# Kernel tuning notes

Measured on AMD Instinct MI355X. Metric: run time of the kernel, lower is better.

Reference implementation:

```python
import jax, jax.numpy as jnp
import numpy as np

BN_EPS = 1e-5


def setup_inputs() -> dict:
    key = jax.random.key(0)
    ks = jax.random.split(key, 6)
    B, N, M, C1, C2 = 8, 8192, 2048, 128, 256
    in_ch = C1 + C2  # 384
    return {
        "xyz1": jax.random.uniform(ks[0], (B, N, 3), dtype=jnp.float32),
        "xyz2": jax.random.uniform(ks[1], (B, M, 3), dtype=jnp.float32),
        "features1": jax.random.normal(ks[2], (B, C1, N), dtype=jnp.float32),
        "features2": jax.random.normal(ks[3], (B, C2, M), dtype=jnp.float32),
        # Conv1d(kernel_size=1, bias=False) weights, squeezed to [out, in]
        "conv_w0": jax.random.normal(ks[4], (256, in_ch), dtype=jnp.float32) * 0.05,
        "gamma0": jnp.ones((256,), dtype=jnp.float32),
        "beta0": jnp.zeros((256,), dtype=jnp.float32),
        "conv_w1": jax.random.normal(ks[5], (256, 256), dtype=jnp.float32) * 0.05,
        "gamma1": jnp.ones((256,), dtype=jnp.float32),
        "beta1": jnp.zeros((256,), dtype=jnp.float32),
    }


def _conv_bn_relu(x, w, gamma, beta):
    # 1x1 Conv1d (no bias) == per-point channel matmul: [B,Cin,N] -> [B,Cout,N]
    x = jnp.einsum("oc,bcn->bon", w, x)
    # BatchNorm1d in training mode: batch stats over (B, N), biased variance
    mu = jnp.mean(x, axis=(0, 2), keepdims=True)
    var = jnp.var(x, axis=(0, 2), keepdims=True)
    x = (x - mu) * jax.lax.rsqrt(var + BN_EPS)
    x = x * gamma[None, :, None] + beta[None, :, None]
    return jax.nn.relu(x)


def reference(xyz1, xyz2, features1, features2,
              conv_w0, gamma0, beta0, conv_w1, gamma1, beta1):
    # squared pairwise distances [B, N, M] (broadcast diff reduced over coord dim)
    diff = xyz1[:, :, None, :] - xyz2[:, None, :, :]  # [B,N,M,3]
    dists = jnp.sum(diff * diff, axis=-1)             # [B,N,M]
    idx = jnp.argmin(dists, axis=-1)                  # [B,N] nearest downsampled point

    # per-batch gather: features2[b, :, idx[b]] -> [B, C2, N]
    interp = jax.vmap(lambda f, i: f[:, i])(features2, idx)

    x = jnp.concatenate([features1, interp], axis=1)  # [B, C1+C2, N]
    x = _conv_bn_relu(x, conv_w0, gamma0, beta0)
    x = _conv_bn_relu(x, conv_w1, gamma1, beta1)
    return x
```

## Files before the change

kernel.cpp:

```cpp
#include <hip/hip_runtime.h>
#include <stdint.h>

typedef unsigned short u16;
typedef unsigned int u32;
typedef __attribute__((ext_vector_type(8))) short short8;
typedef __attribute__((ext_vector_type(4))) float floatx4;

__device__ __forceinline__ u16 f2b(float f) {
  union { float f; u32 u; } c; c.f = f;
  u32 u = c.u;
  u += 0x7fffu + ((u >> 16) & 1u);
  return (u16)(u >> 16);
}
__device__ __forceinline__ float b2f(u16 h) {
  union { u32 u; float f; } c; c.u = ((u32)h) << 16;
  return c.f;
}

__device__ __forceinline__ void glds16(const void* g, void* l) {
  __builtin_amdgcn_global_load_lds((__attribute__((address_space(1))) void*)g,
                                   (__attribute__((address_space(3))) void*)l, 16, 0, 0);
}

__global__ void prep_all_k(const float* __restrict__ xyz1, const float* __restrict__ xyz2,
                           float2* __restrict__ cand,
                           const float* __restrict__ f1, u16* __restrict__ f1t,
                           const float* __restrict__ f2, u16* __restrict__ f2t,
                           const float* __restrict__ w0, u16* __restrict__ w0b,
                           const float* __restrict__ w1, u16* __restrict__ w1b,
                           float* __restrict__ sums) {
  __shared__ __align__(16) char smem[9216];
  int blk = blockIdx.x, t = threadIdx.x;
  if (blk < 512) {
    float4* s2 = (float4*)smem;
    int nq = blk & 7, mq = (blk >> 3) & 7, b = blk >> 6;
    const float* x2 = xyz2 + ((size_t)b * 2048 + mq * 256) * 3;
    s2[t] = make_float4(x2[t * 3], x2[t * 3 + 1], x2[t * 3 + 2], 0.f);
    __syncthreads();
    int n0 = nq * 1024 + t;
    float px[4], py[4], pz[4];
#pragma unroll
    for (int q = 0; q < 4; q++) {
      const float* p1 = xyz1 + ((size_t)b * 8192 + n0 + q * 256) * 3;
      px[q] = p1[0]; py[q] = p1[1]; pz[q] = p1[2];
    }
    float best[4] = {3.0e38f, 3.0e38f, 3.0e38f, 3.0e38f};
    int bi[4] = {0, 0, 0, 0};
#pragma unroll 4
    for (int m = 0; m < 256; m++) {
      float4 qq = s2[m];
#pragma unroll
      for (int q = 0; q < 4; q++) {
        float dx = px[q] - qq.x, dy = py[q] - qq.y, dz = pz[q] - qq.z;
        float d = fmaf(dz, dz, fmaf(dy, dy, dx * dx));
        bool c = d < best[q];
        best[q] = c ? d : best[q];
        bi[q] = c ? m : bi[q];
      }
    }
#pragma unroll
    for (int q = 0; q < 4; q++) {
      int n = n0 + q * 256;
      cand[(size_t)mq * 65536 + (size_t)b * 8192 + n] =
          make_float2(best[q], __int_as_float(mq * 256 + bi[q]));
    }
  } else if (blk < 3584) {
    const float* in; u16* out; int C, N, bx, by, bz;
    if (blk < 2560) { int rel = blk - 512;  in = f1; out = f1t; C = 128; N = 8192; bx = rel & 127; by = (rel >> 7) & 1; bz = rel >> 8; }
    else            { int rel = blk - 2560; in = f2; out = f2t; C = 256; N = 2048; bx = rel & 31;  by = (rel >> 5) & 3; bz = rel >> 7; }
    u16 (*tile)[72] = (u16(*)[72])smem;
    int c0 = by * 64, n0 = bx * 64;
    const float* src = in + ((size_t)bz * C + c0) * N + n0;
#pragma unroll
    for (int i = 0; i < 4; i++) {
      int id = t + i * 256;
      int c = id >> 4, nq = (id & 15) * 4;
      float4 v = *(const float4*)(src + (size_t)c * N + nq);
      tile[nq + 0][c] = f2b(v.x);
      tile[nq + 1][c] = f2b(v.y);
      tile[nq + 2][c] = f2b(v.z);
      tile[nq + 3][c] = f2b(v.w);
    }
    __syncthreads();
    int n = t >> 2, ch = (t & 3) * 16;
    u16* dst = out + ((size_t)bz * N + n0 + n) * C + c0 + ch;
    *(uint4*)dst = *(const uint4*)&tile[n][ch];
    *(uint4*)(dst + 8) = *(const uint4*)&tile[n][ch + 8];
  } else {
    int rel = blk - 3584;
    int i = rel * 256 + t;
    if (rel < 384) w0b[i] = f2b(w0[i]);
    else { int j = i - 98304; w1b[j] = f2b(w1[j]); }
    if (rel < 4) sums[i] = 0.f;
  }
}

__global__ __launch_bounds__(256, 4) void gemm1_k(const u16* __restrict__ w0b, const u16* __restrict__ f1t,
                                                  const u16* __restrict__ f2t, const float2* __restrict__ cand,
                                                  float* __restrict__ sum0, float* __restrict__ sq0,
                                                  u16* __restrict__ y0) {
  __shared__ u16 As[128 * 64];
  __shared__ u16 Bs[128 * 64];
  __shared__ int sidx[128];
  int t = threadIdx.x;
  int ot = blockIdx.x & 1;
  int pt0 = (blockIdx.x >> 1) * 128;
  int o0 = ot * 128;
  int b = pt0 >> 13;
  if (t < 128) {
    int p = pt0 + t;
    float bd = 3.0e38f; int bi = 0;
#pragma unroll
    for (int qc = 0; qc < 8; qc++) {
      float2 c = cand[(size_t)qc * 65536 + p];
      if (c.x < bd) { bd = c.x; bi = __float_as_int(c.y); }
    }
    sidx[t] = bi;
  }
  floatx4 zero = {0.f, 0.f, 0.f, 0.f};
  floatx4 acc[4][4];
#pragma unroll
  for (int i = 0; i < 4; i++)
#pragma unroll
    for (int j = 0; j < 4; j++) acc[i][j] = zero;
  int lane = t & 63, wave = t >> 6;
  int wrow = (wave >> 1) * 64, wcol = (wave & 1) * 64;
  int lr = lane & 15, lq = lane >> 4;
  int srow = lane >> 3;
  int sch = ((lane & 7) ^ srow) * 8;
  __syncthreads();
  int prow[4], gidx[4];
#pragma unroll
  for (int i = 0; i < 4; i++) {
    prow[i] = (wave * 4 + i) * 8 + srow;
    gidx[i] = sidx[prow[i]];
  }

#pragma unroll
  for (int k0 = 0; k0 < 384; k0 += 64) {
    __syncthreads();
#pragma unroll
    for (int i = 0; i < 4; i++) {
      int chunk = wave * 4 + i;
      glds16(w0b + (size_t)(o0 + chunk * 8 + srow) * 384 + k0 + sch, &As[chunk * 512]);
    }
    if (k0 < 128) {
#pragma unroll
      for (int i = 0; i < 4; i++)
        glds16(f1t + (size_t)(pt0 + prow[i]) * 128 + k0 + sch, &Bs[(wave * 4 + i) * 512]);
    } else {
#pragma unroll
      for (int i = 0; i < 4; i++)
        glds16(f2t + ((size_t)(b << 11) + gidx[i]) * 256 + (k0 - 128) + sch, &Bs[(wave * 4 + i) * 512]);
    }
    __syncthreads();
#pragma unroll
    for (int ks = 0; ks < 2; ks++) {
      short8 af[4], bf[4];
#pragma unroll
      for (int i = 0; i < 4; i++) {
        int row = wrow + i * 16 + lr;
        af[i] = *(const short8*)&As[row * 64 + ((((ks << 2) | lq) ^ (lr & 7)) << 3)];
      }
#pragma unroll
      for (int j = 0; j < 4; j++) {
        int row = wcol + j * 16 + lr;
        bf[j] = *(const short8*)&Bs[row * 64 + ((((ks << 2) | lq) ^ (lr & 7)) << 3)];
      }
#pragma unroll
      for (int i = 0; i < 4; i++)
#pragma unroll
        for (int j = 0; j < 4; j++)
          acc[i][j] = __builtin_amdgcn_mfma_f32_16x16x32_bf16(af[i], bf[j], acc[i][j], 0, 0, 0);
    }
  }
#pragma unroll
  for (int i = 0; i < 4; i++) {
#pragma unroll
    for (int j = 0; j < 4; j++) {
      int o = o0 + wrow + i * 16 + lq * 4;
      int p = pt0 + wcol + j * 16 + lr;
      uint2 pk;
      pk.x = (u32)f2b(acc[i][j][0]) | ((u32)f2b(acc[i][j][1]) << 16);
      pk.y = (u32)f2b(acc[i][j][2]) | ((u32)f2b(acc[i][j][3]) << 16);
      *(uint2*)&y0[(size_t)p * 256 + o] = pk;
    }
  }
  __syncthreads();
  float* red = (float*)As;
  red[t] = 0.f;
  __syncthreads();
#pragma unroll
  for (int i = 0; i < 4; i++) {
#pragma unroll
    for (int r = 0; r < 4; r++) {
      float s = acc[i][0][r] + acc[i][1][r] + acc[i][2][r] + acc[i][3][r];
      float q = acc[i][0][r] * acc[i][0][r] + acc[i][1][r] * acc[i][1][r] +
                acc[i][2][r] * acc[i][2][r] + acc[i][3][r] * acc[i][3][r];
#pragma unroll
      for (int m = 8; m >= 1; m >>= 1) { s += __shfl_xor(s, m); q += __shfl_xor(q, m); }
      if (lr == 0) {
        int o = wrow + i * 16 + lq * 4 + r;
        atomicAdd(&red[o], s);
        atomicAdd(&red[128 + o], q);
      }
    }
  }
  __syncthreads();
  if (t < 128) {
    atomicAdd(&sum0[o0 + t], red[t]);
    atomicAdd(&sq0[o0 + t], red[128 + t]);
  }
}

__global__ __launch_bounds__(256, 4) void gemm2_k(const u16* __restrict__ w1b, const u16* __restrict__ y0,
                                                  const float* __restrict__ sum0, const float* __restrict__ sq0,
                                                  const float* __restrict__ gamma0, const float* __restrict__ beta0,
                                                  float* __restrict__ sum1, float* __restrict__ sq1,
                                                  u16* __restrict__ y1) {
  __shared__ u16 As[128 * 64];
  __shared__ u16 Bs[128 * 72];
  __shared__ float ssc[256], ssh[256];
  int t = threadIdx.x;
  {
    float mean = sum0[t] * (1.f / 65536.f);
    float var = fmaxf(sq0[t] * (1.f / 65536.f) - mean * mean, 0.f);
    float r = rsqrtf(var + 1e-5f);
    float sc = gamma0[t] * r;
    ssc[t] = sc;
    ssh[t] = beta0[t] - mean * sc;
  }
  int ot = blockIdx.x & 1;
  int pt0 = (blockIdx.x >> 1) * 128;
  int o0 = ot * 128;
  floatx4 zero = {0.f, 0.f, 0.f, 0.f};
  floatx4 acc[4][4];
#pragma unroll
  for (int i = 0; i < 4; i++)
#pragma unroll
    for (int j = 0; j < 4; j++) acc[i][j] = zero;
  int lane = t & 63, wave = t >> 6;
  int wrow = (wave >> 1) * 64, wcol = (wave & 1) * 64;
  int lr = lane & 15, lq = lane >> 4;
  int srow = lane >> 3;
  int sch = ((lane & 7) ^ srow) * 8;

#pragma unroll
  for (int k0 = 0; k0 < 256; k0 += 64) {
    __syncthreads();
#pragma unroll
    for (int i = 0; i < 4; i++) {
      int chunk = wave * 4 + i;
      glds16(w1b + (size_t)(o0 + chunk * 8 + srow) * 256 + k0 + sch, &As[chunk * 512]);
    }
#pragma unroll
    for (int i = 0; i < 4; i++) {
      int id = t + i * 256;
      int row = id >> 3, ch = (id & 7) * 8;
      uint4 raw = *(const uint4*)(y0 + (size_t)(pt0 + row) * 256 + k0 + ch);
      u32 rw[4] = {raw.x, raw.y, raw.z, raw.w};
      u32 ow[4];
#pragma unroll
      for (int w = 0; w < 4; w++) {
        int k = k0 + ch + w * 2;
        float v0 = b2f((u16)(rw[w] & 0xffffu));
        float v1 = b2f((u16)(rw[w] >> 16));
        v0 = fmaxf(v0 * ssc[k] + ssh[k], 0.f);
        v1 = fmaxf(v1 * ssc[k + 1] + ssh[k + 1], 0.f);
        ow[w] = (u32)f2b(v0) | ((u32)f2b(v1) << 16);
      }
      uint4 ov; ov.x = ow[0]; ov.y = ow[1]; ov.z = ow[2]; ov.w = ow[3];
      *(uint4*)&Bs[row * 72 + ch] = ov;
    }
    __syncthreads();
#pragma unroll
    for (int ks = 0; ks < 2; ks++) {
      int kk = ks * 32 + lq * 8;
      short8 af[4], bf[4];
#pragma unroll
      for (int i = 0; i < 4; i++) {
        int row = wrow + i * 16 + lr;
        af[i] = *(const short8*)&As[row * 64 + ((((ks << 2) | lq) ^ (lr & 7)) << 3)];
      }
#pragma unroll
      for (int j = 0; j < 4; j++) bf[j] = *(const short8*)&Bs[(wcol + j * 16 + lr) * 72 + kk];
#pragma unroll
      for (int i = 0; i < 4; i++)
#pragma unroll
        for (int j = 0; j < 4; j++)
          acc[i][j] = __builtin_amdgcn_mfma_f32_16x16x32_bf16(af[i], bf[j], acc[i][j], 0, 0, 0);
    }
  }
#pragma unroll
  for (int i = 0; i < 4; i++) {
#pragma unroll
    for (int j = 0; j < 4; j++) {
      int o = o0 + wrow + i * 16 + lq * 4;
      int p = pt0 + wcol + j * 16 + lr;
      uint2 pk;
      pk.x = (u32)f2b(acc[i][j][0]) | ((u32)f2b(acc[i][j][1]) << 16);
      pk.y = (u32)f2b(acc[i][j][2]) | ((u32)f2b(acc[i][j][3]) << 16);
      *(uint2*)&y1[(size_t)p * 256 + o] = pk;
    }
  }
  __syncthreads();
  float* red = (float*)As;
  red[t] = 0.f;
  __syncthreads();
#pragma unroll
  for (int i = 0; i < 4; i++) {
#pragma unroll
    for (int r = 0; r < 4; r++) {
      float s = acc[i][0][r] + acc[i][1][r] + acc[i][2][r] + acc[i][3][r];
      float q = acc[i][0][r] * acc[i][0][r] + acc[i][1][r] * acc[i][1][r] +
                acc[i][2][r] * acc[i][2][r] + acc[i][3][r] * acc[i][3][r];
#pragma unroll
      for (int m = 8; m >= 1; m >>= 1) { s += __shfl_xor(s, m); q += __shfl_xor(q, m); }
      if (lr == 0) {
        int o = wrow + i * 16 + lq * 4 + r;
        atomicAdd(&red[o], s);
        atomicAdd(&red[128 + o], q);
      }
    }
  }
  __syncthreads();
  if (t < 128) {
    atomicAdd(&sum1[o0 + t], red[t]);
    atomicAdd(&sq1[o0 + t], red[128 + t]);
  }
}

__global__ void finalize_k(const u16* __restrict__ y1, const float* __restrict__ sum1,
                           const float* __restrict__ sq1, const float* __restrict__ gamma1,
                           const float* __restrict__ beta1, float* __restrict__ out) {
  __shared__ float tile[64][65];
  __shared__ float fs[64], fh[64];
  int b = blockIdx.z, o0 = blockIdx.y * 64, n0 = blockIdx.x * 64;
  int t = threadIdx.x;
  if (t < 64) {
    int o = o0 + t;
    float mean = sum1[o] * (1.f / 65536.f);
    float var = fmaxf(sq1[o] * (1.f / 65536.f) - mean * mean, 0.f);
    float r = rsqrtf(var + 1e-5f);
    float sc = gamma1[o] * r;
    fs[t] = sc;
    fh[t] = beta1[o] - mean * sc;
  }
  __syncthreads();
  int pl = t >> 2, ch = (t & 3) * 16;
  const u16* src = y1 + ((size_t)(b * 8192 + n0 + pl)) * 256 + o0 + ch;
  uint4 r0 = *(const uint4*)src;
  uint4 r1 = *(const uint4*)(src + 8);
  u16 hv[16];
  *(uint4*)&hv[0] = r0;
  *(uint4*)&hv[8] = r1;
#pragma unroll
  for (int e = 0; e < 16; e++) {
    float v = b2f(hv[e]) * fs[ch + e] + fh[ch + e];
    tile[pl][ch + e] = fmaxf(v, 0.f);
  }
  __syncthreads();
  int ol = t >> 2, nch = (t & 3) * 16;
  float* dst = out + ((size_t)(b * 256 + o0 + ol)) * 8192 + n0 + nch;
#pragma unroll
  for (int j = 0; j < 16; j += 4) {
    float4 v = make_float4(tile[nch + j][ol], tile[nch + j + 1][ol],
                           tile[nch + j + 2][ol], tile[nch + j + 3][ol]);
    *(float4*)(dst + j) = v;
  }
}

extern "C" void kernel_launch(void* const* d_in, const int* in_sizes, int n_in,
                              void* d_out, int out_size, void* d_ws, size_t ws_size,
                              hipStream_t stream) {
  const float* xyz1      = (const float*)d_in[0];
  const float* xyz2      = (const float*)d_in[1];
  const float* features1 = (const float*)d_in[2];
  const float* features2 = (const float*)d_in[3];
  const float* conv_w0   = (const float*)d_in[4];
  const float* gamma0    = (const float*)d_in[5];
  const float* beta0     = (const float*)d_in[6];
  const float* conv_w1   = (const float*)d_in[7];
  const float* gamma1    = (const float*)d_in[8];
  const float* beta1     = (const float*)d_in[9];
  float* out = (float*)d_out;

  char* ws = (char*)d_ws;
  size_t off = 0;
  auto alloc = [&](size_t bytes) {
    char* p = ws + off;
    off = (off + bytes + 4095) & ~(size_t)4095;
    return p;
  };
  float*  sums = (float*)alloc(4 * 256 * 4);
  u16*    w0b  = (u16*)alloc(256 * 384 * 2);
  u16*    w1b  = (u16*)alloc(256 * 256 * 2);
  float2* cand = (float2*)alloc((size_t)8 * 65536 * 8);
  u16*    f1t  = (u16*)alloc((size_t)65536 * 128 * 2);
  u16*    f2t  = (u16*)alloc((size_t)16384 * 256 * 2);
  u16*    y0   = (u16*)alloc((size_t)65536 * 256 * 2);
  u16*    y1   = (u16*)alloc((size_t)65536 * 256 * 2);

  prep_all_k<<<dim3(4224), 256, 0, stream>>>(xyz1, xyz2, cand, features1, f1t,
                                             features2, f2t, conv_w0, w0b, conv_w1, w1b, sums);
  gemm1_k<<<dim3(1024), 256, 0, stream>>>(w0b, f1t, f2t, cand, sums + 0, sums + 256, y0);
  gemm2_k<<<dim3(1024), 256, 0, stream>>>(w1b, y0, sums + 0, sums + 256, gamma0, beta0,
                                          sums + 512, sums + 768, y1);
  finalize_k<<<dim3(128, 4, 8), 256, 0, stream>>>(y1, sums + 512, sums + 768, gamma1, beta1, out);
}
```

Measured before the change: 239.3 us.

## Keep weight slice resident in LDS and loop blocks over point tiles with double buffering

Both GEMM kernels now load their full 128-row weight slice into LDS once per block and iterate over several point tiles (persistent-style, 256 blocks of 512 threads), so weights are no longer re-fetched for every K step of every tile. B tiles are double-buffered so the next K slice loads while the current one computes, and in gemm2 the BN+ReLU transform of y0 is split into register prefetch and LDS write to overlap with MFMA. BN partial sums are accumulated in registers across tiles and reduced once per block, which cuts atomics. The costs are large LDS use (about 128 KB in gemm2), which limits occupancy, and only 256 blocks, which may underfill the device.

```diff
diff --git a/kernel.cpp b/kernel.cpp
--- a/kernel.cpp
+++ b/kernel.cpp
@@ -95,116 +95,148 @@
   }
 }
 
-__global__ __launch_bounds__(256, 4) void gemm1_k(const u16* __restrict__ w0b, const u16* __restrict__ f1t,
+__global__ __launch_bounds__(512, 2) void gemm1_k(const u16* __restrict__ w0b, const u16* __restrict__ f1t,
                                                   const u16* __restrict__ f2t, const float2* __restrict__ cand,
                                                   float* __restrict__ sum0, float* __restrict__ sq0,
                                                   u16* __restrict__ y0) {
-  __shared__ u16 As[128 * 64];
-  __shared__ u16 Bs[128 * 64];
-  __shared__ int sidx[128];
+  __shared__ u16 Aw[128 * 384];
+  __shared__ u16 Bs[2][128 * 64];
   int t = threadIdx.x;
-  int ot = blockIdx.x & 1;
-  int pt0 = (blockIdx.x >> 1) * 128;
-  int o0 = ot * 128;
-  int b = pt0 >> 13;
-  if (t < 128) {
-    int p = pt0 + t;
-    float bd = 3.0e38f; int bi = 0;
-#pragma unroll
-    for (int qc = 0; qc < 8; qc++) {
-      float2 c = cand[(size_t)qc * 65536 + p];
-      if (c.x < bd) { bd = c.x; bi = __float_as_int(c.y); }
-    }
-    sidx[t] = bi;
-  }
-  floatx4 zero = {0.f, 0.f, 0.f, 0.f};
-  floatx4 acc[4][4];
-#pragma unroll
-  for (int i = 0; i < 4; i++)
-#pragma unroll
-    for (int j = 0; j < 4; j++) acc[i][j] = zero;
+  int bid = blockIdx.x;
+  int ohalf = (bid >> 3) & 1;
+  int pairidx = (bid & 7) | ((bid >> 4) << 3);
+  int o0 = ohalf * 128;
   int lane = t & 63, wave = t >> 6;
-  int wrow = (wave >> 1) * 64, wcol = (wave & 1) * 64;
+  int wrow = (wave >> 2) * 64;
+  int wp = (wave & 3) * 32;
   int lr = lane & 15, lq = lane >> 4;
   int srow = lane >> 3;
   int sch = ((lane & 7) ^ srow) * 8;
-  __syncthreads();
-  int prow[4], gidx[4];
-#pragma unroll
-  for (int i = 0; i < 4; i++) {
-    prow[i] = (wave * 4 + i) * 8 + srow;
-    gidx[i] = sidx[prow[i]];
-  }
-
-#pragma unroll
-  for (int k0 = 0; k0 < 384; k0 += 64) {
+
+#pragma unroll
+  for (int it = 0; it < 12; it++) {
+    u32 off = (u32)it * 8192 + (u32)t * 16;
+    int row = off / 768;
+    int c16 = (off - row * 768) >> 4;
+    glds16(w0b + (size_t)(o0 + row) * 384 + ((c16 ^ (row & 7)) << 3),
+           (char*)Aw + (size_t)it * 8192 + (size_t)wave * 1024);
+  }
+
+  float sa[4][4], qa[4][4];
+#pragma unroll
+  for (int i = 0; i < 4; i++)
+#pragma unroll
+    for (int r = 0; r < 4; r++) { sa[i][r] = 0.f; qa[i][r] = 0.f; }
+
+  for (int s = 0; s < 4; s++) {
+    int pt = pairidx * 4 + s;
+    int pt0 = pt * 128;
+    int b = pt0 >> 13;
+    int gidx[2];
+#pragma unroll
+    for (int i = 0; i < 2; i++) {
+      int p = pt0 + (wave * 2 + i) * 8 + srow;
+      float bd = 3.0e38f; int bi = 0;
+#pragma unroll
+      for (int qc = 0; qc < 8; qc++) {
+        float2 c = cand[(size_t)qc * 65536 + p];
+        if (c.x < bd) { bd = c.x; bi = __float_as_int(c.y); }
+      }
+      gidx[i] = bi;
+    }
+    floatx4 zero = {0.f, 0.f, 0.f, 0.f};
+    floatx4 acc[4][2];
+#pragma unroll
+    for (int i = 0; i < 4; i++)
+#pragma unroll
+      for (int j = 0; j < 2; j++) acc[i][j] = zero;
+
+    auto stageB = [&](int k0, int bufi) {
+      if (k0 < 128) {
+#pragma unroll
+        for (int i = 0; i < 2; i++)
+          glds16(f1t + (size_t)(pt0 + (wave * 2 + i) * 8 + srow) * 128 + k0 + sch,
+                 &Bs[bufi][(wave * 2 + i) * 512]);
+      } else {
+#pragma unroll
+        for (int i = 0; i < 2; i++)
+          glds16(f2t + ((size_t)(b << 11) + gidx[i]) * 256 + (k0 - 128) + sch,
+                 &Bs[bufi][(wave * 2 + i) * 512]);
+      }
+    };
+    auto compute = [&](int k0, int bufi) {
+#pragma unroll
+      for (int ks = 0; ks < 2; ks++) {
+        short8 af[4], bf[2];
+#pragma unroll
+        for (int i = 0; i < 4; i++) {
+          int row = wrow + i * 16 + lr;
+          af[i] = *(const short8*)&Aw[row * 384 + ((((k0 >> 3) + (ks << 2) + lq) ^ (lr & 7)) << 3)];
+        }
+#pragma unroll
+        for (int j = 0; j < 2; j++) {
+          int row = wp + j * 16 + lr;
+          bf[j] = *(const short8*)&Bs[bufi][row * 64 + ((((ks << 2) | lq) ^ (lr & 7)) << 3)];
+        }
+#pragma unroll
+        for (int i = 0; i < 4; i++)
+#pragma unroll
+          for (int j = 0; j < 2; j++)
+            acc[i][j] = __builtin_amdgcn_mfma_f32_16x16x32_bf16(af[i], bf[j], acc[i][j], 0, 0, 0);
+      }
+    };
+
+    stageB(0, 0);
     __syncthreads();
 #pragma unroll
+    for (int k0i = 0; k0i < 6; k0i++) {
+      if (k0i < 5) stageB((k0i + 1) * 64, (k0i + 1) & 1);
+      compute(k0i * 64, k0i & 1);
+      __syncthreads();
+    }
+
+#pragma unroll
     for (int i = 0; i < 4; i++) {
-      int chunk = wave * 4 + i;
-      glds16(w0b + (size_t)(o0 + chunk * 8 + srow) * 384 + k0 + sch, &As[chunk * 512]);
-    }
-    if (k0 < 128) {
-#pragma unroll
-      for (int i = 0; i < 4; i++)
-        glds16(f1t + (size_t)(pt0 + prow[i]) * 128 + k0 + sch, &Bs[(wave * 4 + i) * 512]);
-    } else {
-#pragma unroll
-      for (int i = 0; i < 4; i++)
-        glds16(f2t + ((size_t)(b << 11) + gidx[i]) * 256 + (k0 - 128) + sch, &Bs[(wave * 4 + i) * 512]);
-    }
-    __syncthreads();
-#pragma unroll
-    for (int ks = 0; ks < 2; ks++) {
-      short8 af[4], bf[4];
-#pragma unroll
-      for (int i = 0; i < 4; i++) {
-        int row = wrow + i * 16 + lr;
-        af[i] = *(const short8*)&As[row * 64 + ((((ks << 2) | lq) ^ (lr & 7)) << 3)];
-      }
-#pragma unroll
-      for (int j = 0; j < 4; j++) {
-        int row = wcol + j * 16 + lr;
-        bf[j] = *(const short8*)&Bs[row * 64 + ((((ks << 2) | lq) ^ (lr & 7)) << 3)];
-      }
-#pragma unroll
-      for (int i = 0; i < 4; i++)
-#pragma unroll
-        for (int j = 0; j < 4; j++)
-          acc[i][j] = __builtin_amdgcn_mfma_f32_16x16x32_bf16(af[i], bf[j], acc[i][j], 0, 0, 0);
-    }
-  }
-#pragma unroll
-  for (int i = 0; i < 4; i++) {
-#pragma unroll
-    for (int j = 0; j < 4; j++) {
-      int o = o0 + wrow + i * 16 + lq * 4;
-      int p = pt0 + wcol + j * 16 + lr;
-      uint2 pk;
-      pk.x = (u32)f2b(acc[i][j][0]) | ((u32)f2b(acc[i][j][1]) << 16);
-      pk.y = (u32)f2b(acc[i][j][2]) | ((u32)f2b(acc[i][j][3]) << 16);
-      *(uint2*)&y0[(size_t)p * 256 + o] = pk;
-    }
-  }
-  __syncthreads();
-  float* red = (float*)As;
-  red[t] = 0.f;
-  __syncthreads();
-#pragma unroll
-  for (int i = 0; i < 4; i++) {
-#pragma unroll
-    for (int r = 0; r < 4; r++) {
-      float s = acc[i][0][r] + acc[i][1][r] + acc[i][2][r] + acc[i][3][r];
-      float q = acc[i][0][r] * acc[i][0][r] + acc[i][1][r] * acc[i][1][r] +
-                acc[i][2][r] * acc[i][2][r] + acc[i][3][r] * acc[i][3][r];
-#pragma unroll
-      for (int m = 8; m >= 1; m >>= 1) { s += __shfl_xor(s, m); q += __shfl_xor(q, m); }
-      if (lr == 0) {
+#pragma unroll
+      for (int j = 0; j < 2; j++) {
+        int o = o0 + wrow + i * 16 + lq * 4;
+        int p = pt0 + wp + j * 16 + lr;
+        uint2 pk;
+        pk.x = (u32)f2b(acc[i][j][0]) | ((u32)f2b(acc[i][j][1]) << 16);
+        pk.y = (u32)f2b(acc[i][j][2]) | ((u32)f2b(acc[i][j][3]) << 16);
+        *(uint2*)&y0[(size_t)p * 256 + o] = pk;
+      }
+#pragma unroll
+      for (int r = 0; r < 4; r++) {
+        float v0 = acc[i][0][r], v1 = acc[i][1][r];
+        sa[i][r] += v0 + v1;
+        qa[i][r] += v0 * v0 + v1 * v1;
+      }
+    }
+  }
+
+#pragma unroll
+  for (int i = 0; i < 4; i++)
+#pragma unroll
+    for (int r = 0; r < 4; r++)
+#pragma unroll
+      for (int m = 8; m >= 1; m >>= 1) {
+        sa[i][r] += __shfl_xor(sa[i][r], m);
+        qa[i][r] += __shfl_xor(qa[i][r], m);
+      }
+  __syncthreads();
+  float* red = (float*)&Bs[0][0];
+  if (t < 256) red[t] = 0.f;
+  __syncthreads();
+  if (lr == 0) {
+#pragma unroll
+    for (int i = 0; i < 4; i++)
+#pragma unroll
+      for (int r = 0; r < 4; r++) {
         int o = wrow + i * 16 + lq * 4 + r;
-        atomicAdd(&red[o], s);
-        atomicAdd(&red[128 + o], q);
-      }
-    }
+        atomicAdd(&red[o], sa[i][r]);
+        atomicAdd(&red[128 + o], qa[i][r]);
+      }
   }
   __syncthreads();
   if (t < 128) {
@@ -213,16 +245,24 @@
   }
 }
 
-__global__ __launch_bounds__(256, 4) void gemm2_k(const u16* __restrict__ w1b, const u16* __restrict__ y0,
+__global__ __launch_bounds__(512, 2) void gemm2_k(const u16* __restrict__ w1b, const u16* __restrict__ y0,
                                                   const float* __restrict__ sum0, const float* __restrict__ sq0,
                                                   const float* __restrict__ gamma0, const float* __restrict__ beta0,
                                                   float* __restrict__ sum1, float* __restrict__ sq1,
                                                   u16* __restrict__ y1) {
-  __shared__ u16 As[128 * 64];
-  __shared__ u16 Bs[128 * 72];
+  __shared__ u16 Aw[128 * 256];
+  __shared__ u16 Bs[2][256 * 64];
   __shared__ float ssc[256], ssh[256];
   int t = threadIdx.x;
-  {
+  int bid = blockIdx.x;
+  int ohalf = (bid >> 3) & 1;
+  int pairidx = (bid & 7) | ((bid >> 4) << 3);
+  int o0 = ohalf * 128;
+  int lane = t & 63, wave = t >> 6;
+  int wrow = (wave >> 2) * 64;
+  int wp = (wave & 3) * 64;
+  int lr = lane & 15, lq = lane >> 4;
+  if (t < 256) {
     float mean = sum0[t] * (1.f / 65536.f);
     float var = fmaxf(sq0[t] * (1.f / 65536.f) - mean * mean, 0.f);
     float r = rsqrtf(var + 1e-5f);
@@ -230,98 +270,139 @@
     ssc[t] = sc;
     ssh[t] = beta0[t] - mean * sc;
   }
-  int ot = blockIdx.x & 1;
-  int pt0 = (blockIdx.x >> 1) * 128;
-  int o0 = ot * 128;
-  floatx4 zero = {0.f, 0.f, 0.f, 0.f};
-  floatx4 acc[4][4];
+#pragma unroll
+  for (int it = 0; it < 8; it++) {
+    u32 off = (u32)it * 8192 + (u32)t * 16;
+    int row = off >> 9;
+    int c16 = (off & 511) >> 4;
+    glds16(w1b + (size_t)(o0 + row) * 256 + ((c16 ^ (row & 7)) << 3),
+           (char*)Aw + (size_t)it * 8192 + (size_t)wave * 1024);
+  }
+
+  int brow[4], bpc[4], bch[4];
+#pragma unroll
+  for (int i = 0; i < 4; i++) {
+    int id = t + i * 512;
+    brow[i] = id >> 3; bpc[i] = id & 7;
+    bch[i] = (bpc[i] ^ (brow[i] & 7)) * 8;
+  }
+  float sa[4][4], qa[4][4];
 #pragma unroll
   for (int i = 0; i < 4; i++)
 #pragma unroll
-    for (int j = 0; j < 4; j++) acc[i][j] = zero;
-  int lane = t & 63, wave = t >> 6;
-  int wrow = (wave >> 1) * 64, wcol = (wave & 1) * 64;
-  int lr = lane & 15, lq = lane >> 4;
-  int srow = lane >> 3;
-  int sch = ((lane & 7) ^ srow) * 8;
-
-#pragma unroll
-  for (int k0 = 0; k0 < 256; k0 += 64) {
+    for (int r = 0; r < 4; r++) { sa[i][r] = 0.f; qa[i][r] = 0.f; }
+
+  __syncthreads();
+
+  for (int s = 0; s < 2; s++) {
+    int pt0 = (pairidx * 2 + s) * 256;
+    uint4 rg[4];
+    auto loadB = [&](int k0) {
+#pragma unroll
+      for (int i = 0; i < 4; i++)
+        rg[i] = *(const uint4*)(y0 + (size_t)(pt0 + brow[i]) * 256 + k0 + bch[i]);
+    };
+    auto xformB = [&](int k0, int bufi) {
+#pragma unroll
+      for (int i = 0; i < 4; i++) {
+        u32 rw[4] = {rg[i].x, rg[i].y, rg[i].z, rg[i].w};
+        u32 ow[4];
+#pragma unroll
+        for (int w = 0; w < 4; w++) {
+          int k = k0 + bch[i] + w * 2;
+          float v0 = b2f((u16)(rw[w] & 0xffffu));
+          float v1 = b2f((u16)(rw[w] >> 16));
+          v0 = fmaxf(v0 * ssc[k] + ssh[k], 0.f);
+          v1 = fmaxf(v1 * ssc[k + 1] + ssh[k + 1], 0.f);
+          ow[w] = (u32)f2b(v0) | ((u32)f2b(v1) << 16);
+        }
+        uint4 ov; ov.x = ow[0]; ov.y = ow[1]; ov.z = ow[2]; ov.w = ow[3];
+        *(uint4*)&Bs[bufi][brow[i] * 64 + bpc[i] * 8] = ov;
+      }
+    };
+    floatx4 zero = {0.f, 0.f, 0.f, 0.f};
+    floatx4 acc[4][4];
+#pragma unroll
+    for (int i = 0; i < 4; i++)
+#pragma unroll
+      for (int j = 0; j < 4; j++) acc[i][j] = zero;
+    auto compute = [&](int k0, int bufi) {
+#pragma unroll
+      for (int ks = 0; ks < 2; ks++) {
+        short8 af[4], bf[4];
+#pragma unroll
+        for (int i = 0; i < 4; i++) {
+          int row = wrow + i * 16 + lr;
+          af[i] = *(const short8*)&Aw[row * 256 + ((((k0 >> 3) + (ks << 2) + lq) ^ (lr & 7)) << 3)];
+        }
+#pragma unroll
+        for (int j = 0; j < 4; j++) {
+          int row = wp + j * 16 + lr;
+          bf[j] = *(const short8*)&Bs[bufi][row * 64 + ((((ks << 2) | lq) ^ (lr & 7)) << 3)];
+        }
+#pragma unroll
+        for (int i = 0; i < 4; i++)
+#pragma unroll
+          for (int j = 0; j < 4; j++)
+            acc[i][j] = __builtin_amdgcn_mfma_f32_16x16x32_bf16(af[i], bf[j], acc[i][j], 0, 0, 0);
+      }
+    };
+
+    loadB(0);
+    xformB(0, 0);
     __syncthreads();
 #pragma unroll
+    for (int k0i = 0; k0i < 4; k0i++) {
+      if (k0i < 3) loadB((k0i + 1) * 64);
+      compute(k0i * 64, k0i & 1);
+      __syncthreads();
+      if (k0i < 3) {
+        xformB((k0i + 1) * 64, (k0i + 1) & 1);
+        __syncthreads();
+      }
+    }
+#pragma unroll
     for (int i = 0; i < 4; i++) {
-      int chunk = wave * 4 + i;
-      glds16(w1b + (size_t)(o0 + chunk * 8 + srow) * 256 + k0 + sch, &As[chunk * 512]);
-    }
-#pragma unroll
-    for (int i = 0; i < 4; i++) {
-      int id = t + i * 256;
-      int row = id >> 3, ch = (id & 7) * 8;
-      uint4 raw = *(const uint4*)(y0 + (size_t)(pt0 + row) * 256 + k0 + ch);
-      u32 rw[4] = {raw.x, raw.y, raw.z, raw.w};
-      u32 ow[4];
-#pragma unroll
-      for (int w = 0; w < 4; w++) {
-        int k = k0 + ch + w * 2;
-        float v0 = b2f((u16)(rw[w] & 0xffffu));
-        float v1 = b2f((u16)(rw[w] >> 16));
-        v0 = fmaxf(v0 * ssc[k] + ssh[k], 0.f);
-        v1 = fmaxf(v1 * ssc[k + 1] + ssh[k + 1], 0.f);
-        ow[w] = (u32)f2b(v0) | ((u32)f2b(v1) << 16);
-      }
-      uint4 ov; ov.x = ow[0]; ov.y = ow[1]; ov.z = ow[2]; ov.w = ow[3];
-      *(uint4*)&Bs[row * 72 + ch] = ov;
-    }
-    __syncthreads();
-#pragma unroll
-    for (int ks = 0; ks < 2; ks++) {
-      int kk = ks * 32 + lq * 8;
-      short8 af[4], bf[4];
-#pragma unroll
-      for (int i = 0; i < 4; i++) {
-        int row = wrow + i * 16 + lr;
-        af[i] = *(const short8*)&As[row * 64 + ((((ks << 2) | lq) ^ (lr & 7)) << 3)];
-      }
-#pragma unroll
-      for (int j = 0; j < 4; j++) bf[j] = *(const short8*)&Bs[(wcol + j * 16 + lr) * 72 + kk];
-#pragma unroll
-      for (int i = 0; i < 4; i++)
-#pragma unroll
-        for (int j = 0; j < 4; j++)
-          acc[i][j] = __builtin_amdgcn_mfma_f32_16x16x32_bf16(af[i], bf[j], acc[i][j], 0, 0, 0);
-    }
-  }
-#pragma unroll
-  for (int i = 0; i < 4; i++) {
-#pragma unroll
-    for (int j = 0; j < 4; j++) {
-      int o = o0 + wrow + i * 16 + lq * 4;
-      int p = pt0 + wcol + j * 16 + lr;
-      uint2 pk;
-      pk.x = (u32)f2b(acc[i][j][0]) | ((u32)f2b(acc[i][j][1]) << 16);
-      pk.y = (u32)f2b(acc[i][j][2]) | ((u32)f2b(acc[i][j][3]) << 16);
-      *(uint2*)&y1[(size_t)p * 256 + o] = pk;
-    }
-  }
-  __syncthreads();
-  float* red = (float*)As;
-  red[t] = 0.f;
-  __syncthreads();
-#pragma unroll
-  for (int i = 0; i < 4; i++) {
-#pragma unroll
-    for (int r = 0; r < 4; r++) {
-      float s = acc[i][0][r] + acc[i][1][r] + acc[i][2][r] + acc[i][3][r];
-      float q = acc[i][0][r] * acc[i][0][r] + acc[i][1][r] * acc[i][1][r] +
-                acc[i][2][r] * acc[i][2][r] + acc[i][3][r] * acc[i][3][r];
-#pragma unroll
-      for (int m = 8; m >= 1; m >>= 1) { s += __shfl_xor(s, m); q += __shfl_xor(q, m); }
-      if (lr == 0) {
+#pragma unroll
+      for (int j = 0; j < 4; j++) {
+        int o = o0 + wrow + i * 16 + lq * 4;
+        int p = pt0 + wp + j * 16 + lr;
+        uint2 pk;
+        pk.x = (u32)f2b(acc[i][j][0]) | ((u32)f2b(acc[i][j][1]) << 16);
+        pk.y = (u32)f2b(acc[i][j][2]) | ((u32)f2b(acc[i][j][3]) << 16);
+        *(uint2*)&y1[(size_t)p * 256 + o] = pk;
+      }
+#pragma unroll
+      for (int r = 0; r < 4; r++) {
+        float v0 = acc[i][0][r], v1 = acc[i][1][r], v2 = acc[i][2][r], v3 = acc[i][3][r];
+        sa[i][r] += v0 + v1 + v2 + v3;
+        qa[i][r] += v0 * v0 + v1 * v1 + v2 * v2 + v3 * v3;
+      }
+    }
+  }
+
+#pragma unroll
+  for (int i = 0; i < 4; i++)
+#pragma unroll
+    for (int r = 0; r < 4; r++)
+#pragma unroll
+      for (int m = 8; m >= 1; m >>= 1) {
+        sa[i][r] += __shfl_xor(sa[i][r], m);
+        qa[i][r] += __shfl_xor(qa[i][r], m);
+      }
+  __syncthreads();
+  float* red = (float*)&Bs[0][0];
+  if (t < 256) red[t] = 0.f;
+  __syncthreads();
+  if (lr == 0) {
+#pragma unroll
+    for (int i = 0; i < 4; i++)
+#pragma unroll
+      for (int r = 0; r < 4; r++) {
         int o = wrow + i * 16 + lq * 4 + r;
-        atomicAdd(&red[o], s);
-        atomicAdd(&red[128 + o], q);
-      }
-    }
+        atomicAdd(&red[o], sa[i][r]);
+        atomicAdd(&red[128 + o], qa[i][r]);
+      }
   }
   __syncthreads();
   if (t < 128) {
@@ -403,8 +484,8 @@
 
   prep_all_k<<<dim3(4224), 256, 0, stream>>>(xyz1, xyz2, cand, features1, f1t,
                                              features2, f2t, conv_w0, w0b, conv_w1, w1b, sums);
-  gemm1_k<<<dim3(1024), 256, 0, stream>>>(w0b, f1t, f2t, cand, sums + 0, sums + 256, y0);
-  gemm2_k<<<dim3(1024), 256, 0, stream>>>(w1b, y0, sums + 0, sums + 256, gamma0, beta0,
-                                          sums + 512, sums + 768, y1);
+  gemm1_k<<<dim3(256), 512, 0, stream>>>(w0b, f1t, f2t, cand, sums + 0, sums + 256, y0);
+  gemm2_k<<<dim3(256), 512, 0, stream>>>(w1b, y0, sums + 0, sums + 256, gamma0, beta0,
+                                         sums + 512, sums + 768, y1);
   finalize_k<<<dim3(128, 4, 8), 256, 0, stream>>>(y1, sums + 512, sums + 768, gamma1, beta1, out);
 }
```

Measured after the change: 231.2 us. 1.03x faster.
